# Kernel optimization log

Measured on AMD Instinct MI355X. Metric: run time of the kernel, lower is better.

The kernel has to match this reference:

```python
import jax, jax.numpy as jnp
import numpy as np
from jax import lax


def _conv3d(x, w, b, circular=False):
    # x: (B,C,D,H,W), w: (O,I,kd,kh,kw)
    if circular:
        x = jnp.pad(x, ((0, 0), (0, 0), (1, 1), (1, 1), (1, 1)), mode='wrap')
    y = lax.conv_general_dilated(x, w, (1, 1, 1), 'VALID',
                                 dimension_numbers=('NCDHW', 'OIDHW', 'NCDHW'))
    return y + b[None, :, None, None, None]


def _inorm(x):
    # InstanceNorm3d, affine=False, eps=1e-5, biased variance over spatial dims
    mu = jnp.mean(x, axis=(2, 3, 4), keepdims=True)
    var = jnp.var(x, axis=(2, 3, 4), keepdims=True)
    return (x - mu) * lax.rsqrt(var + 1e-5)


def _gelu(x):
    return jax.nn.gelu(x, approximate=False)


def _r6_to_matrix(r6):
    eps = 1e-7
    v1 = r6[..., :3]
    v1 = v1 / (jnp.linalg.norm(v1, axis=-1, keepdims=True) + eps)
    v2 = r6[..., 3:]
    v2 = v2 - jnp.sum(v2 * v1, -1, keepdims=True) * v1
    v2 = v2 / (jnp.linalg.norm(v2, axis=-1, keepdims=True) + eps)
    v3 = jnp.cross(v1, v2)
    det = jnp.linalg.det(jnp.stack([v1, v2, v3], axis=-2))
    v3 = jnp.where(det[..., None] < 0, -v3, v3)
    return jnp.stack([v1, v2, v3], axis=-2)


def _ensure_matrix(R):
    def fnorm(v):
        return v / jnp.maximum(jnp.linalg.norm(v, axis=-1, keepdims=True), 1e-12)
    v1 = fnorm(R[..., 0, :] + 1e-6)
    v2 = R[..., 1, :]
    v2 = fnorm(v2 - jnp.sum(v2 * v1, -1, keepdims=True) * v1 + 1e-6)
    v3 = jnp.cross(v1, v2)
    det = jnp.linalg.det(jnp.stack([v1, v2, v3], axis=-2))
    v3 = jnp.where(det[..., None] < 0, -v3, v3)
    Rn = jnp.stack([v1, v2, v3], axis=-2)
    Rt = jnp.swapaxes(Rn, -2, -1)
    return 0.5 * (Rn + Rt @ Rn @ Rt)


def _rotate(X, R):
    # X: (bd, nh, L, hd); R: (nh, 3, 3). Pads hd to a multiple of 3, rotates
    # each 3-vector group by R^T-on-the-right (X_rot = X @ R^T).
    hd = X.shape[-1]
    pad = (-hd) % 3
    Xp = jnp.pad(X, ((0, 0), (0, 0), (0, 0), (0, pad))) if pad else X
    nv = Xp.shape[-1] // 3
    Xr = Xp.reshape(Xp.shape[:-1] + (nv, 3))
    Y = jnp.einsum('bhlvi,hji->bhlvj', Xr, R).reshape(Xp.shape)
    return Y[..., :hd] if pad else Y


def _forward(x, pos_emb, qkv_w, qkv_b, lp_w1, lp_b1, lp_w2, lp_b2,
             mod_w1, mod_b1, mod_w2, mod_b2, pa_w, pa_b,
             proj_w, proj_b, pos_bias_w, pos_bias_b,
             A_d, A_h, A_w, R_d, R_h, R_w, t_d, t_h, t_w):
    B, C, D, H, W = x.shape
    nh = pa_w.shape[0]
    hd = C // nh
    scale = hd ** -0.5

    # PositionalProcessing (identical for all three axial passes)
    lf = _conv3d(pos_emb, lp_w1, lp_b1, circular=True)
    lf = _conv3d(_gelu(_inorm(lf)), lp_w2, lp_b2)
    m = _conv3d(lf, mod_w1, mod_b1)
    m = jax.nn.sigmoid(_conv3d(_gelu(_inorm(m)), mod_w2, mod_b2))
    x_mod = x * m                                   # (B,C,D,H,W)
    pa = _gelu(_inorm(_conv3d(pos_emb, pa_w, pa_b)))  # (B,nh,D,H,W)

    def axial(comp, perm, inv_perm, A, R, t):
        xp = jnp.transpose(x_mod, perm)             # (B, a, b, C, L)
        Bp, a, b, _, L = xp.shape
        bd = Bp * a * b
        xf = jnp.swapaxes(xp.reshape(bd, C, L), 1, 2)  # (bd, L, C)
        qkv = (xf @ qkv_w.T + qkv_b).reshape(bd, L, 3, nh, hd)
        qkv = jnp.transpose(qkv, (2, 0, 3, 1, 4))
        q, k, v = qkv[0], qkv[1], qkv[2]
        R_qk = _r6_to_matrix(A[0].astype(jnp.float32))  # (nh,3,3), same for all bd
        R_v = _ensure_matrix(R[0])                      # (nh,3,3)
        q_r, k_r, v_r = _rotate(q, R_qk), _rotate(k, R_qk), _rotate(v, R_v)
        # axis positions: linspace on one coordinate component
        pos = jnp.zeros((L, 3), x.dtype).at[:, comp].set(jnp.linspace(-1.0, 1.0, L))
        pos_t = pos[None] + t[0]                        # (nh, L, 3)
        rel = pos_t[:, :, None, :] - pos_t[:, None, :, :]  # (nh, L, L, 3)
        bias = jnp.einsum('hqkc,c->hqk', rel, pos_bias_w[0]) + pos_bias_b[0]
        pa_p = jnp.transpose(pa, perm).reshape(bd, nh, L)
        attn = jnp.einsum('bhqd,bhkd->bhqk', q_r, k_r) * scale
        attn = jax.nn.softmax(attn + pa_p[..., None] + bias[None], axis=-1)
        out = jnp.einsum('bhqk,bhkd->bhqd', attn, v_r)
        out = jnp.transpose(out, (0, 2, 1, 3)).reshape(Bp, a, b, L, C)
        return jnp.transpose(out, inv_perm)             # back to (B,C,D,H,W)

    out = (axial(2, (0, 3, 4, 1, 2), (0, 4, 3, 1, 2), A_d, R_d, t_d)
           + axial(1, (0, 2, 4, 1, 3), (0, 4, 1, 3, 2), A_h, R_h, t_h)
           + axial(0, (0, 2, 3, 1, 4), (0, 4, 1, 2, 3), A_w, R_w, t_w))
    return jnp.einsum('oc,bcdhw->bodhw', proj_w[:, :, 0, 0, 0], out) + proj_b[None, :, None, None, None]


def setup_inputs() -> dict:
    key = jax.random.key(0)
    B, C, D, H, W, nh = 2, 128, 32, 32, 32, 8
    ks = jax.random.split(key, 24)

    def n(k, shape, s=0.05):
        return (jax.random.normal(k, shape) * s).astype(jnp.float32)

    def r6(k):
        k1, k2 = jax.random.split(k)
        v1 = jax.random.normal(k1, (1, nh, 3))
        v1 = v1 / jnp.linalg.norm(v1, axis=-1, keepdims=True)
        v2 = jax.random.normal(k2, (1, nh, 3))
        v2 = v2 - jnp.sum(v2 * v1, -1, keepdims=True) * v1
        v2 = v2 / jnp.linalg.norm(v2, axis=-1, keepdims=True)
        return jnp.concatenate([v1, v2], -1).astype(jnp.float32)

    eye = jnp.broadcast_to(jnp.eye(3, dtype=jnp.float32), (1, nh, 3, 3))
    return {
        'x': jax.random.normal(ks[0], (B, C, D, H, W), jnp.float32),
        'pos_emb': jax.random.normal(ks[1], (B, C, D, H, W), jnp.float32),
        'qkv_w': n(ks[2], (3 * C, C)), 'qkv_b': n(ks[3], (3 * C,)),
        'lp_w1': n(ks[4], (C, C, 3, 3, 3), 0.02), 'lp_b1': n(ks[5], (C,)),
        'lp_w2': n(ks[6], (C, C, 1, 1, 1)), 'lp_b2': n(ks[7], (C,)),
        'mod_w1': n(ks[8], (C, C, 1, 1, 1)), 'mod_b1': n(ks[9], (C,)),
        'mod_w2': n(ks[10], (C, C, 1, 1, 1)), 'mod_b2': n(ks[11], (C,)),
        'pa_w': n(ks[12], (nh, C, 1, 1, 1)), 'pa_b': n(ks[13], (nh,)),
        'proj_w': n(ks[14], (C, C, 1, 1, 1)), 'proj_b': n(ks[15], (C,)),
        'pos_bias_w': n(ks[16], (1, 3), 0.5), 'pos_bias_b': n(ks[17], (1,)),
        'A_d': r6(ks[18]), 'A_h': r6(ks[19]), 'A_w': r6(ks[20]),
        'R_d': eye, 'R_h': eye, 'R_w': eye,
        't_d': n(ks[21], (1, nh, 1, 3), 0.01),
        't_h': n(ks[22], (1, nh, 1, 3), 0.01),
        't_w': n(ks[23], (1, nh, 1, 3), 0.01),
    }


def reference(x, pos_emb, qkv_w, qkv_b, lp_w1, lp_b1, lp_w2, lp_b2,
              mod_w1, mod_b1, mod_w2, mod_b2, pa_w, pa_b,
              proj_w, proj_b, pos_bias_w, pos_bias_b,
              A_d, A_h, A_w, R_d, R_h, R_w, t_d, t_h, t_w):
    return _forward(x, pos_emb, qkv_w, qkv_b, lp_w1, lp_b1, lp_w2, lp_b2,
                    mod_w1, mod_b1, mod_w2, mod_b2, pa_w, pa_b,
                    proj_w, proj_b, pos_bias_w, pos_bias_b,
                    A_d, A_h, A_w, R_d, R_h, R_w, t_d, t_h, t_w)
```

## Files before the change

kernel.cpp:

```cpp
#include <hip/hip_runtime.h>
#include <cstdint>
#include <cstddef>


#define NTOK 65536
#define SPAT 32768

#define WS_R0     0ull
#define WS_A0     0ull
#define WS_A1     4194304ull
#define WS_MPREB  8388608ull
#define WS_A2     8388608ull
#define WS_XTOKB  12582912ull
#define WS_INT    16777216ull
#define WS_QKVH   20971520ull
#define WS_CONVP  33554432ull
#define WS_QKVP   33775616ull
#define WS_WCP    33800192ull
#define WS_MODW2P 33808384ull
#define WS_PROJP  33816576ull
#define WS_BC     33824768ull
#define WS_RBUF   33824896ull
#define WS_PS     33825328ull
#define WS_PSS    33956400ull
#define WS_MU1    34087472ull
#define WS_RS1    34087728ull
#define WS_MU2    34087984ull
#define WS_RS2    34088240ull

typedef __attribute__((ext_vector_type(8))) short short8;
typedef __attribute__((ext_vector_type(4))) float f32x4;
typedef __attribute__((ext_vector_type(16))) float f32x16;

__device__ __forceinline__ float gelu_f(float x) {
  float u = 0.79788456080286536f * (x + 0.044715f * x * x * x);
  u = fminf(u, 40.0f);
  float e = __expf(2.0f * u);
  float t = (e - 1.0f) / (e + 1.0f);
  return 0.5f * x * (1.0f + t);
}
__device__ __forceinline__ float sigmoid_f(float x) {
  return 1.0f / (1.0f + __expf(-x));
}
__device__ __forceinline__ unsigned short f2bf(float x) {
  unsigned int u = __float_as_uint(x);
  unsigned int r = u + 0x7fffu + ((u >> 16) & 1u);
  return (unsigned short)(r >> 16);
}
__device__ __forceinline__ float bf2f(unsigned short u) {
  return __uint_as_float(((unsigned int)u) << 16);
}
__device__ __forceinline__ void bf16x16_load(const unsigned short* p, float* f) {
  const uint4 a = *(const uint4*)p;
  const uint4 b = *(const uint4*)(p + 8);
  const unsigned int w[8] = {a.x, a.y, a.z, a.w, b.x, b.y, b.z, b.w};
  #pragma unroll
  for (int i = 0; i < 8; ++i) {
    f[2 * i] = __uint_as_float(w[i] << 16);
    f[2 * i + 1] = __uint_as_float(w[i] & 0xffff0000u);
  }
}
__device__ __forceinline__ void bf16x8_load(const unsigned short* p, float* f) {
  const uint4 a = *(const uint4*)p;
  const unsigned int w[4] = {a.x, a.y, a.z, a.w};
  #pragma unroll
  for (int i = 0; i < 4; ++i) {
    f[2 * i] = __uint_as_float(w[i] << 16);
    f[2 * i + 1] = __uint_as_float(w[i] & 0xffff0000u);
  }
}
__device__ __forceinline__ void gload_lds16(const void* g, void* l) {
  __builtin_amdgcn_global_load_lds(
      (const __attribute__((address_space(1))) unsigned int*)g,
      (__attribute__((address_space(3))) unsigned int*)l, 16, 0, 0);
}
__device__ __forceinline__ float dot3(const float* a, const float* b) {
  return a[0] * b[0] + a[1] * b[1] + a[2] * b[2];
}
__device__ __forceinline__ void cross3(const float* a, const float* b, float* c) {
  c[0] = a[1] * b[2] - a[2] * b[1];
  c[1] = a[2] * b[0] - a[0] * b[2];
  c[2] = a[0] * b[1] - a[1] * b[0];
}

__device__ void r6_to_matrix(const float* r6, float* R) {
  float v1[3] = {r6[0], r6[1], r6[2]};
  float n1 = sqrtf(dot3(v1, v1));
  float inv1 = 1.0f / (n1 + 1e-7f);
  v1[0] *= inv1; v1[1] *= inv1; v1[2] *= inv1;
  float v2[3] = {r6[3], r6[4], r6[5]};
  float d = dot3(v2, v1);
  v2[0] -= d * v1[0]; v2[1] -= d * v1[1]; v2[2] -= d * v1[2];
  float n2 = sqrtf(dot3(v2, v2));
  float inv2 = 1.0f / (n2 + 1e-7f);
  v2[0] *= inv2; v2[1] *= inv2; v2[2] *= inv2;
  float v3[3]; cross3(v1, v2, v3);
  float cx[3]; cross3(v2, v3, cx);
  float det = dot3(v1, cx);
  if (det < 0.0f) { v3[0] = -v3[0]; v3[1] = -v3[1]; v3[2] = -v3[2]; }
  R[0] = v1[0]; R[1] = v1[1]; R[2] = v1[2];
  R[3] = v2[0]; R[4] = v2[1]; R[5] = v2[2];
  R[6] = v3[0]; R[7] = v3[1]; R[8] = v3[2];
}

__device__ void ensure_matrix(const float* Rin, float* Ro) {
  float a[3] = {Rin[0] + 1e-6f, Rin[1] + 1e-6f, Rin[2] + 1e-6f};
  float na = fmaxf(sqrtf(dot3(a, a)), 1e-12f);
  float v1[3] = {a[0] / na, a[1] / na, a[2] / na};
  float b0[3] = {Rin[3], Rin[4], Rin[5]};
  float d = dot3(b0, v1);
  float bb[3] = {b0[0] - d * v1[0] + 1e-6f, b0[1] - d * v1[1] + 1e-6f, b0[2] - d * v1[2] + 1e-6f};
  float nb = fmaxf(sqrtf(dot3(bb, bb)), 1e-12f);
  float v2[3] = {bb[0] / nb, bb[1] / nb, bb[2] / nb};
  float v3[3]; cross3(v1, v2, v3);
  float cx[3]; cross3(v2, v3, cx);
  float det = dot3(v1, cx);
  if (det < 0.0f) { v3[0] = -v3[0]; v3[1] = -v3[1]; v3[2] = -v3[2]; }
  float Rn[9] = {v1[0], v1[1], v1[2], v2[0], v2[1], v2[2], v3[0], v3[1], v3[2]};
  float T1[9], T2[9];
  for (int i = 0; i < 3; ++i)
    for (int j = 0; j < 3; ++j) {
      float s = 0.f;
      for (int k = 0; k < 3; ++k) s += Rn[k * 3 + i] * Rn[k * 3 + j];
      T1[i * 3 + j] = s;
    }
  for (int i = 0; i < 3; ++i)
    for (int j = 0; j < 3; ++j) {
      float s = 0.f;
      for (int k = 0; k < 3; ++k) s += T1[i * 3 + k] * Rn[j * 3 + k];
      T2[i * 3 + j] = s;
    }
  for (int i = 0; i < 9; ++i) Ro[i] = 0.5f * (Rn[i] + T2[i]);
}

__device__ __forceinline__ void rot16(const float* R, const float* x, float* y) {
  #pragma unroll
  for (int g = 0; g < 5; ++g) {
    float a = x[3 * g], b = x[3 * g + 1], c = x[3 * g + 2];
    y[3 * g + 0] = R[0] * a + R[1] * b + R[2] * c;
    y[3 * g + 1] = R[3] * a + R[4] * b + R[5] * c;
    y[3 * g + 2] = R[6] * a + R[7] * b + R[8] * c;
  }
  y[15] = R[0] * x[15];
}

__global__ __launch_bounds__(256) void prep_transpose_kernel(
    const float* __restrict__ lp_w1, const float* __restrict__ qkv_w,
    const float* __restrict__ mod_w1, const float* __restrict__ lp_w2,
    const float* __restrict__ lp_b2, const float* __restrict__ mod_b1,
    const float* __restrict__ mod_w2, const float* __restrict__ proj_w,
    const float* __restrict__ Ad, const float* __restrict__ Ah,
    const float* __restrict__ Aw, const float* __restrict__ Rd,
    const float* __restrict__ Rh, const float* __restrict__ Rw,
    const float* __restrict__ x, const float* __restrict__ pe,
    unsigned short* __restrict__ convP, unsigned short* __restrict__ qkvP,
    unsigned short* __restrict__ WcP, unsigned short* __restrict__ modw2P,
    unsigned short* __restrict__ projP, float* __restrict__ bc,
    float* __restrict__ Rbuf, unsigned short* __restrict__ xtokb,
    unsigned short* __restrict__ inT) {
  __shared__ float lds[32][132];
  if (blockIdx.x < 256) {
    int gid = blockIdx.x * 256 + threadIdx.x;
    for (int f = gid; f < 442368; f += 65536) {
      int e = f & 7;
      int co = (f >> 3) & 127;
      int rest = f >> 10;
      int l4 = rest & 3;
      int ks = (rest >> 2) & 3;
      int dxt = rest >> 4;
      int dx = dxt % 3;
      int tap = dxt / 3;
      int dz = tap / 3, dy = tap % 3;
      int ci = ks * 32 + l4 * 8 + e;
      convP[f] = f2bf(lp_w1[(co * 128 + ci) * 27 + dz * 9 + dy * 3 + dx]);
    }
    if (gid < 49152) qkvP[gid] = f2bf(qkv_w[gid]);
    if (gid < 16384) {
      modw2P[gid] = f2bf(mod_w2[gid]);
      projP[gid] = f2bf(proj_w[gid]);
      int o = gid >> 7, i = gid & 127;
      float s = 0.f;
      for (int c = 0; c < 128; ++c) s += mod_w1[o * 128 + c] * lp_w2[c * 128 + i];
      WcP[gid] = f2bf(s);
    }
    if (gid < 128) {
      float s = 0.f;
      for (int c = 0; c < 128; ++c) s += mod_w1[gid * 128 + c] * lp_b2[c];
      bc[gid] = s + mod_b1[gid];
    }
    if (blockIdx.x == 0 && threadIdx.x >= 224 && threadIdx.x < 248) {
      int tid = threadIdx.x - 224;
      int ax = tid >> 3, h = tid & 7;
      const float* A = (ax == 0) ? Ad : ((ax == 1) ? Ah : Aw);
      const float* R = (ax == 0) ? Rd : ((ax == 1) ? Rh : Rw);
      float Rq[9], Rv[9];
      r6_to_matrix(A + h * 6, Rq);
      ensure_matrix(R + h * 9, Rv);
      float* dst = Rbuf + (ax * 8 + h) * 18;
      for (int i = 0; i < 9; ++i) { dst[i] = Rq[i]; dst[9 + i] = Rv[i]; }
    }
    return;
  }
  int blk = blockIdx.x - 256;
  int b = blk >> 10;
  int dh = blk & 1023;
  int tid = threadIdx.x;
  size_t planebase = ((size_t)b << 22) + ((size_t)dh << 5);
  size_t tb = ((size_t)blk) << 5;
  #pragma unroll
  for (int r = 0; r < 16; ++r) {
    int idx = r * 256 + tid;
    int ci = idx >> 5, w = idx & 31;
    lds[w][ci] = x[planebase + ((size_t)ci << 15) + w];
  }
  __syncthreads();
  #pragma unroll
  for (int r = 0; r < 16; ++r) {
    int idx = r * 256 + tid;
    int w = idx >> 7, ci = idx & 127;
    xtokb[(tb + w) * 128 + ci] = f2bf(lds[w][ci]);
  }
  __syncthreads();
  #pragma unroll
  for (int r = 0; r < 16; ++r) {
    int idx = r * 256 + tid;
    int ci = idx >> 5, w = idx & 31;
    lds[w][ci] = pe[planebase + ((size_t)ci << 15) + w];
  }
  __syncthreads();
  #pragma unroll
  for (int r = 0; r < 16; ++r) {
    int idx = r * 256 + tid;
    int w = idx >> 7, ci = idx & 127;
    inT[(tb + w) * 128 + ci] = f2bf(lds[w][ci]);
  }
}

__global__ __launch_bounds__(256, 4) void conv_mfma_kernel(
    const unsigned short* __restrict__ inT, const unsigned short* __restrict__ Bp,
    const float* __restrict__ b1, unsigned short* __restrict__ out,
    float* __restrict__ ps, float* __restrict__ pss) {
  __shared__ unsigned short Als[16384];
  __shared__ float sumb[128];
  __shared__ float sqb[128];
  const int orig = blockIdx.x;
  const int blk = ((orig & 7) << 7) + (orig >> 3);
  const int b = blk >> 9, d = (blk >> 4) & 31, hg = blk & 15;
  const int h0 = hg << 1;
  const int tid = threadIdx.x;
  const int lane = tid & 63;
  const int wid = tid >> 6;
  const int l15 = lane & 15, l4 = lane >> 4;

  f32x4 acc[4][2];
  #pragma unroll
  for (int mt = 0; mt < 4; ++mt)
    #pragma unroll
    for (int nt = 0; nt < 2; ++nt)
      #pragma unroll
      for (int r = 0; r < 4; ++r) acc[mt][nt][r] = 0.f;

  int mw[4], mhh[4];
  #pragma unroll
  for (int mt = 0; mt < 4; ++mt) {
    int m = mt * 16 + l15;
    mhh[mt] = m >> 5;
    mw[mt] = m & 31;
  }
  const size_t tokbase = ((size_t)b << 15) + ((size_t)d << 10) + ((size_t)h0 << 5);

  auto stage = [&](int dz) {
    const int zr = (d + dz + 31) & 31;
    #pragma unroll
    for (int p = 0; p < 8; ++p) {
      const int g = p * 256 + tid;
      const int tok = g >> 4, gi = g & 15;
      const int r = tok >> 5, w = tok & 31;
      const int yr = (h0 + r + 31) & 31;
      const size_t srcbyte = ((((size_t)b << 15) + ((size_t)zr << 10) + ((size_t)yr << 5) + w) << 8)
                             + (size_t)((gi ^ (w & 7)) << 4);
      gload_lds16((const char*)inT + srcbyte, (char*)Als + (size_t)g * 16);
    }
  };

  auto compute = [&](int dz) {
    #pragma unroll
    for (int dy = 0; dy < 3; ++dy) {
      const int tap = dz * 3 + dy;
      #pragma unroll
      for (int dx = 0; dx < 3; ++dx) {
        int abase[4], asw[4];
        #pragma unroll
        for (int mt = 0; mt < 4; ++mt) {
          const int wsft = (mw[mt] + dx + 31) & 31;
          const int stok = (mhh[mt] + dy) * 32 + wsft;
          abase[mt] = stok * 256;
          asw[mt] = (wsft & 7) << 4;
        }
        #pragma unroll
        for (int ks = 0; ks < 4; ++ks) {
          const int k2 = (ks * 32 + l4 * 8) * 2;
          const int bbase = (((tap * 3 + dx) * 4 + ks) * 4 + l4) * 1024;
          short8 afr[4], bfr[2];
          #pragma unroll
          for (int nt = 0; nt < 2; ++nt) {
            const int co = wid * 32 + nt * 16 + l15;
            bfr[nt] = *(const short8*)(Bp + bbase + co * 8);
          }
          #pragma unroll
          for (int mt = 0; mt < 4; ++mt)
            afr[mt] = *(const short8*)((const char*)Als + abase[mt] + (k2 ^ asw[mt]));
          __builtin_amdgcn_s_setprio(1);
          #pragma unroll
          for (int mt = 0; mt < 4; ++mt)
            #pragma unroll
            for (int nt = 0; nt < 2; ++nt)
              acc[mt][nt] = __builtin_amdgcn_mfma_f32_16x16x32_bf16(afr[mt], bfr[nt],
                                                                    acc[mt][nt], 0, 0, 0);
          __builtin_amdgcn_s_setprio(0);
        }
      }
    }
  };

  for (int dz = 0; dz < 3; ++dz) {
    stage(dz);
    __syncthreads();
    compute(dz);
    if (dz < 2) __syncthreads();
  }

  #pragma unroll
  for (int nt = 0; nt < 2; ++nt) {
    const int co = wid * 32 + nt * 16 + l15;
    const float bias = b1[co];
    float s = 0.f, q = 0.f;
    #pragma unroll
    for (int mt = 0; mt < 4; ++mt) {
      #pragma unroll
      for (int r = 0; r < 4; ++r) {
        const int m = mt * 16 + l4 * 4 + r;
        const float v = acc[mt][nt][r] + bias;
        out[(tokbase + m) * 128 + co] = f2bf(v);
        s += v; q += v * v;
      }
    }
    s += __shfl_xor(s, 16); s += __shfl_xor(s, 32);
    q += __shfl_xor(q, 16); q += __shfl_xor(q, 32);
    if (l4 == 0) { sumb[co] = s; sqb[co] = q; }
  }
  __syncthreads();
  if (tid < 128) {
    ps[blk * 128 + tid] = sumb[tid];
    pss[blk * 128 + tid] = sqb[tid];
  }
}

__global__ __launch_bounds__(64) void stats_final_kernel(
    const float* __restrict__ ps, const float* __restrict__ pss,
    float* __restrict__ mu, float* __restrict__ rs, int nb) {
  const int pair = blockIdx.x;
  const int b = pair >> 7, c = pair & 127;
  const int lane = threadIdx.x;
  float s = 0.f, ss = 0.f;
  for (int j = lane; j < nb; j += 64) {
    const int idx = ((b * nb + j) << 7) + c;
    s += ps[idx];
    ss += pss[idx];
  }
  #pragma unroll
  for (int o = 32; o > 0; o >>= 1) {
    s += __shfl_xor(s, o);
    ss += __shfl_xor(ss, o);
  }
  if (lane == 0) {
    float m = s * (1.0f / 32768.0f);
    float v = ss * (1.0f / 32768.0f) - m * m;
    mu[pair] = m;
    rs[pair] = rsqrtf(v + 1e-5f);
  }
}

template <int PRE, int AB16, int POST, int STATS>
__global__ __launch_bounds__(256) void gemm_mfma_kernel(
    const void* __restrict__ Avoid, const unsigned short* __restrict__ Wp,
    const float* __restrict__ bias, void* __restrict__ Yvoid, int O,
    const float* __restrict__ mu, const float* __restrict__ rs,
    const unsigned short* __restrict__ xtb, float* __restrict__ ps,
    float* __restrict__ pss) {
  __shared__ float sumb[128][2];
  __shared__ float sqb[128][2];
  const int tid = threadIdx.x;
  const int lane = tid & 63, wid = tid >> 6;
  const int wm = wid >> 1, wn = wid & 1;
  const int l15 = lane & 15, l4 = lane >> 4;
  const int og = blockIdx.x * 128;
  const int t0 = blockIdx.y * 128;
  const int bidx = t0 >> 15;
  const float* Af = (const float*)Avoid;
  const unsigned short* Ab = (const unsigned short*)Avoid;
  float* Yf = (float*)Yvoid;
  unsigned short* Yb = (unsigned short*)Yvoid;

  f32x4 acc[4][4];
  #pragma unroll
  for (int mt = 0; mt < 4; ++mt)
    #pragma unroll
    for (int nt = 0; nt < 4; ++nt)
      #pragma unroll
      for (int r = 0; r < 4; ++r) acc[mt][nt][r] = 0.f;

  #pragma unroll
  for (int ks = 0; ks < 4; ++ks) {
    const int kb = ks * 32 + l4 * 8;
    short8 a[4], bfr[4];
    float4 m0, m1, r0, r1;
    if constexpr (PRE == 1) {
      m0 = *(const float4*)(mu + bidx * 128 + kb);
      m1 = *(const float4*)(mu + bidx * 128 + kb + 4);
      r0 = *(const float4*)(rs + bidx * 128 + kb);
      r1 = *(const float4*)(rs + bidx * 128 + kb + 4);
    }
    #pragma unroll
    for (int mt = 0; mt < 4; ++mt) {
      const int tok = t0 + wm * 64 + mt * 16 + l15;
      float v[16];
      bool have = false;
      if constexpr (AB16 == 1) {
        if constexpr (PRE == 1) {
          bf16x16_load(Ab + (size_t)tok * 128 + kb, v);
          have = true;
        } else {
          a[mt] = *(const short8*)(Ab + (size_t)tok * 128 + kb);
        }
      } else {
        const float* ap = Af + (size_t)tok * 128 + kb;
        float4 v0 = *(const float4*)ap;
        float4 v1 = *(const float4*)(ap + 4);
        v[0] = v0.x; v[1] = v0.y; v[2] = v0.z; v[3] = v0.w;
        v[4] = v1.x; v[5] = v1.y; v[6] = v1.z; v[7] = v1.w;
        have = true;
      }
      if (have) {
        if constexpr (PRE == 1) {
          const float mm[8] = {m0.x, m0.y, m0.z, m0.w, m1.x, m1.y, m1.z, m1.w};
          const float rr[8] = {r0.x, r0.y, r0.z, r0.w, r1.x, r1.y, r1.z, r1.w};
          #pragma unroll
          for (int j = 0; j < 8; ++j) v[j] = gelu_f((v[j] - mm[j]) * rr[j]);
        }
        short8 t;
        #pragma unroll
        for (int j = 0; j < 8; ++j) t[j] = (short)f2bf(v[j]);
        a[mt] = t;
      }
    }
    #pragma unroll
    for (int nt = 0; nt < 4; ++nt) {
      const int o = og + wn * 64 + nt * 16 + l15;
      bfr[nt] = *(const short8*)(Wp + (size_t)o * 128 + kb);
    }
    #pragma unroll
    for (int mt = 0; mt < 4; ++mt)
      #pragma unroll
      for (int nt = 0; nt < 4; ++nt)
        acc[mt][nt] = __builtin_amdgcn_mfma_f32_16x16x32_bf16(a[mt], bfr[nt], acc[mt][nt], 0, 0, 0);
  }

  #pragma unroll
  for (int nt = 0; nt < 4; ++nt) {
    const int o = og + wn * 64 + nt * 16 + l15;
    const float bb = bias[o];
    float s = 0.f, q = 0.f;
    #pragma unroll
    for (int mt = 0; mt < 4; ++mt) {
      #pragma unroll
      for (int r = 0; r < 4; ++r) {
        const int t = t0 + wm * 64 + mt * 16 + l4 * 4 + r;
        const float v = acc[mt][nt][r] + bb;
        if constexpr (POST == 0) {
          Yf[(size_t)t * O + o] = v;
        } else if constexpr (POST == 2) {
          Yb[(size_t)t * O + o] = f2bf(v);
        }
        if constexpr (STATS) { s += v; q += v * v; }
      }
    }
    if constexpr (STATS) {
      s += __shfl_xor(s, 16); s += __shfl_xor(s, 32);
      q += __shfl_xor(q, 16); q += __shfl_xor(q, 32);
      if (l4 == 0) { sumb[o - og][wm] = s; sqb[o - og][wm] = q; }
    }
  }
  if constexpr (STATS) {
    __syncthreads();
    if (tid < 128) {
      ps[blockIdx.y * 128 + tid] = sumb[tid][0] + sumb[tid][1];
      pss[blockIdx.y * 128 + tid] = sqb[tid][0] + sqb[tid][1];
    }
  }
}

__global__ __launch_bounds__(256) void gateqkv_mfma_kernel(
    const unsigned short* __restrict__ mpreb, const unsigned short* __restrict__ modw2P,
    const float* __restrict__ mod_b2, const unsigned short* __restrict__ xtb,
    const unsigned short* __restrict__ qkvP, const float* __restrict__ qkv_b,
    unsigned short* __restrict__ qkvt, const float* __restrict__ mu,
    const float* __restrict__ rs) {
  __shared__ char ga[32768];
  __shared__ char xm[32768];
  const int tid = threadIdx.x;
  const int lane = tid & 63, wid = tid >> 6;
  const int wm = wid >> 1, wn = wid & 1;
  const int l15 = lane & 15, l4 = lane >> 4;
  const int t0 = blockIdx.x * 128;
  const int bidx = t0 >> 15;

  #pragma unroll
  for (int r = 0; r < 8; ++r) {
    const int c = r * 256 + tid;
    const int tl = c >> 4;
    const int kc = (c & 15) * 8;
    float v[8];
    bf16x8_load(mpreb + (size_t)(t0 + tl) * 128 + kc, v);
    const float4 m0 = *(const float4*)(mu + bidx * 128 + kc);
    const float4 m1 = *(const float4*)(mu + bidx * 128 + kc + 4);
    const float4 r0 = *(const float4*)(rs + bidx * 128 + kc);
    const float4 r1 = *(const float4*)(rs + bidx * 128 + kc + 4);
    const float mm[8] = {m0.x, m0.y, m0.z, m0.w, m1.x, m1.y, m1.z, m1.w};
    const float rr[8] = {r0.x, r0.y, r0.z, r0.w, r1.x, r1.y, r1.z, r1.w};
    short8 t;
    #pragma unroll
    for (int j = 0; j < 8; ++j) t[j] = (short)f2bf(gelu_f((v[j] - mm[j]) * rr[j]));
    *(short8*)(ga + tl * 256 + ((kc * 2) ^ ((tl & 7) << 4))) = t;
  }
  __syncthreads();

  f32x4 acc[4][4];
  #pragma unroll
  for (int mt = 0; mt < 4; ++mt)
    #pragma unroll
    for (int nt = 0; nt < 4; ++nt)
      #pragma unroll
      for (int r = 0; r < 4; ++r) acc[mt][nt][r] = 0.f;

  #pragma unroll
  for (int ks = 0; ks < 4; ++ks) {
    const int kb = ks * 32 + l4 * 8;
    short8 a[4], bfr[4];
    #pragma unroll
    for (int mt = 0; mt < 4; ++mt) {
      const int tl = wm * 64 + mt * 16 + l15;
      a[mt] = *(const short8*)(ga + tl * 256 + ((kb * 2) ^ ((tl & 7) << 4)));
    }
    #pragma unroll
    for (int nt = 0; nt < 4; ++nt) {
      const int o = wn * 64 + nt * 16 + l15;
      bfr[nt] = *(const short8*)(modw2P + (size_t)o * 128 + kb);
    }
    #pragma unroll
    for (int mt = 0; mt < 4; ++mt)
      #pragma unroll
      for (int nt = 0; nt < 4; ++nt)
        acc[mt][nt] = __builtin_amdgcn_mfma_f32_16x16x32_bf16(a[mt], bfr[nt], acc[mt][nt], 0, 0, 0);
  }
  #pragma unroll
  for (int nt = 0; nt < 4; ++nt) {
    const int o = wn * 64 + nt * 16 + l15;
    const float bb = mod_b2[o];
    #pragma unroll
    for (int mt = 0; mt < 4; ++mt) {
      #pragma unroll
      for (int r = 0; r < 4; ++r) {
        const int tl = wm * 64 + mt * 16 + l4 * 4 + r;
        const int t = t0 + tl;
        const float v = sigmoid_f(acc[mt][nt][r] + bb) * bf2f(xtb[(size_t)t * 128 + o]);
        *(unsigned short*)(xm + tl * 256 + ((o * 2) ^ ((tl & 7) << 4))) = f2bf(v);
      }
    }
  }
  __syncthreads();

  for (int c = 0; c < 3; ++c) {
    #pragma unroll
    for (int mt = 0; mt < 4; ++mt)
      #pragma unroll
      for (int nt = 0; nt < 4; ++nt)
        #pragma unroll
        for (int r = 0; r < 4; ++r) acc[mt][nt][r] = 0.f;
    #pragma unroll
    for (int ks = 0; ks < 4; ++ks) {
      const int kb = ks * 32 + l4 * 8;
      short8 a[4], bfr[4];
      #pragma unroll
      for (int mt = 0; mt < 4; ++mt) {
        const int tl = wm * 64 + mt * 16 + l15;
        a[mt] = *(const short8*)(xm + tl * 256 + ((kb * 2) ^ ((tl & 7) << 4)));
      }
      #pragma unroll
      for (int nt = 0; nt < 4; ++nt) {
        const int o = c * 128 + wn * 64 + nt * 16 + l15;
        bfr[nt] = *(const short8*)(qkvP + (size_t)o * 128 + kb);
      }
      #pragma unroll
      for (int mt = 0; mt < 4; ++mt)
        #pragma unroll
        for (int nt = 0; nt < 4; ++nt)
          acc[mt][nt] = __builtin_amdgcn_mfma_f32_16x16x32_bf16(a[mt], bfr[nt], acc[mt][nt], 0, 0, 0);
    }
    #pragma unroll
    for (int nt = 0; nt < 4; ++nt) {
      const int o = c * 128 + wn * 64 + nt * 16 + l15;
      const float bb = qkv_b[o];
      const int hsub = (o & 127) >> 4, ch = o & 15;
      #pragma unroll
      for (int mt = 0; mt < 4; ++mt) {
        #pragma unroll
        for (int r = 0; r < 4; ++r) {
          const int t = t0 + wm * 64 + mt * 16 + l4 * 4 + r;
          qkvt[(size_t)t * 384 + hsub * 48 + c * 16 + ch] = f2bf(acc[mt][nt][r] + bb);
        }
      }
    }
  }
}

__global__ __launch_bounds__(256) void proj_mfma_kernel(
    const unsigned short* __restrict__ A0b, const unsigned short* __restrict__ A1b,
    const unsigned short* __restrict__ A2b, const unsigned short* __restrict__ Wp,
    const float* __restrict__ bias, float* __restrict__ out) {
  const int tid = threadIdx.x;
  const int lane = tid & 63, wid = tid >> 6;
  const int wm = wid >> 1, wn = wid & 1;
  const int l15 = lane & 15, l4 = lane >> 4;
  const int t0 = blockIdx.x * 128;

  f32x4 acc[4][4];
  #pragma unroll
  for (int mt = 0; mt < 4; ++mt)
    #pragma unroll
    for (int nt = 0; nt < 4; ++nt)
      #pragma unroll
      for (int r = 0; r < 4; ++r) acc[mt][nt][r] = 0.f;

  #pragma unroll
  for (int ks = 0; ks < 4; ++ks) {
    const int kb = ks * 32 + l4 * 8;
    short8 a[4], bfr[4];
    #pragma unroll
    for (int mt = 0; mt < 4; ++mt) {
      const int o = wm * 64 + mt * 16 + l15;
      a[mt] = *(const short8*)(Wp + (size_t)o * 128 + kb);
    }
    #pragma unroll
    for (int nt = 0; nt < 4; ++nt) {
      const int tok = t0 + wn * 64 + nt * 16 + l15;
      const size_t off = (size_t)tok * 128 + kb;
      short8 s0 = *(const short8*)(A0b + off);
      short8 s1 = *(const short8*)(A1b + off);
      short8 s2 = *(const short8*)(A2b + off);
      short8 r;
      #pragma unroll
      for (int i = 0; i < 8; ++i) {
        float f = bf2f((unsigned short)s0[i]) + bf2f((unsigned short)s1[i]) +
                  bf2f((unsigned short)s2[i]);
        r[i] = (short)f2bf(f);
      }
      bfr[nt] = r;
    }
    #pragma unroll
    for (int mt = 0; mt < 4; ++mt)
      #pragma unroll
      for (int nt = 0; nt < 4; ++nt)
        acc[mt][nt] = __builtin_amdgcn_mfma_f32_16x16x32_bf16(a[mt], bfr[nt], acc[mt][nt], 0, 0, 0);
  }

  #pragma unroll
  for (int nt = 0; nt < 4; ++nt) {
    const int tok = t0 + wn * 64 + nt * 16 + l15;
    const int dhw = tok & 32767, bB = tok >> 15;
    #pragma unroll
    for (int mt = 0; mt < 4; ++mt) {
      #pragma unroll
      for (int r = 0; r < 4; ++r) {
        const int o = wm * 64 + mt * 16 + l4 * 4 + r;
        out[((size_t)(bB * 128 + o) << 15) + dhw] = acc[mt][nt][r] + bias[o];
      }
    }
  }
}

__global__ __launch_bounds__(512) void attn_mfma_kernel(
    const unsigned short* __restrict__ qkvt, const float* __restrict__ Rbuf,
    const float* __restrict__ pbw, unsigned short* __restrict__ a0,
    unsigned short* __restrict__ a1, unsigned short* __restrict__ a2) {
  __shared__ unsigned short rows[32 * 392];
  __shared__ unsigned short Vt[8][16 * 40];
  __shared__ float Ot[8][32 * 20];
  const int axial = blockIdx.y;
  const int seq = blockIdx.x;
  unsigned short* dstbuf = (axial == 0) ? a0 : ((axial == 1) ? a1 : a2);
  const int tid = threadIdx.x;
  const int lane = tid & 63, head = tid >> 6;
  const int tok = lane & 31, hi = lane >> 5;
  const int b = seq >> 10, rem = seq & 1023;
  const int u = rem >> 5, v = rem & 31;
  int base, stride, comp;
  if (axial == 0)      { base = (b << 15) + (u << 5) + v;         stride = 1024; comp = 2; }
  else if (axial == 1) { base = (b << 15) + (u << 10) + v;        stride = 32;   comp = 1; }
  else                 { base = (b << 15) + (u << 10) + (v << 5); stride = 1;    comp = 0; }

  #pragma unroll
  for (int p = 0; p < 3; ++p) {
    const int c = p * 512 + tid;
    const int r = c / 48, cw = c - r * 48;
    const size_t src = ((size_t)base + (size_t)r * stride) * 384 + (size_t)cw * 8;
    *(uint4*)((char*)rows + r * 784 + cw * 16) = *(const uint4*)(qkvt + src);
  }
  __syncthreads();

  const float* Rp = Rbuf + (axial * 8 + head) * 18;
  const float rq00 = fabsf(Rp[0]);
  const unsigned short* myrow = rows + tok * 392 + head * 48;
  short8 aq = *(const short8*)(myrow + hi * 8);
  short8 ak = *(const short8*)(myrow + 16 + hi * 8);
  short8 av = *(const short8*)(myrow + 32 + hi * 8);
  if (hi) {
    aq[7] = (short)f2bf(bf2f((unsigned short)aq[7]) * rq00);
    ak[7] = (short)f2bf(bf2f((unsigned short)ak[7]) * rq00);
  }
  #pragma unroll
  for (int e = 0; e < 8; ++e) Vt[head][(hi * 8 + e) * 40 + tok] = (unsigned short)av[e];

  f32x16 sacc;
  #pragma unroll
  for (int r = 0; r < 16; ++r) sacc[r] = 0.f;
  sacc = __builtin_amdgcn_mfma_f32_32x32x16_bf16(ak, aq, sacc, 0, 0, 0);
  const float wb = pbw[comp];
  float p[16];
  float mmax = -1e30f;
  #pragma unroll
  for (int r = 0; r < 16; ++r) {
    const int kk = (r & 3) + 4 * hi + 8 * (r >> 2);
    const float lin = -1.0f + (2.0f / 31.0f) * (float)kk;
    p[r] = sacc[r] * 0.25f - lin * wb;
    mmax = fmaxf(mmax, p[r]);
  }
  mmax = fmaxf(mmax, __shfl_xor(mmax, 32));
  float sum = 0.f;
  #pragma unroll
  for (int r = 0; r < 16; ++r) { p[r] = expf(p[r] - mmax); sum += p[r]; }
  sum += __shfl_xor(sum, 32);
  const float inv = 1.0f / sum;
  #pragma unroll
  for (int r = 0; r < 16; ++r) p[r] *= inv;
  unsigned pk[8], sw[8];
  #pragma unroll
  for (int j = 0; j < 8; ++j) {
    unsigned r_;
    asm("v_cvt_pk_bf16_f32 %0, %1, %2" : "=v"(r_) : "v"(p[2 * j]), "v"(p[2 * j + 1]));
    pk[j] = r_;
  }
  #pragma unroll
  for (int j = 0; j < 8; ++j) sw[j] = (unsigned)__shfl_xor((int)pk[j], 32);
  uint4 Fu, Gu;
  Fu.x = hi ? sw[2] : pk[0];
  Fu.y = hi ? sw[3] : pk[1];
  Fu.z = hi ? pk[2] : sw[0];
  Fu.w = hi ? pk[3] : sw[1];
  Gu.x = hi ? sw[6] : pk[4];
  Gu.y = hi ? sw[7] : pk[5];
  Gu.z = hi ? pk[6] : sw[4];
  Gu.w = hi ? pk[7] : sw[5];
  short8 Pf = *(short8*)&Fu;
  short8 Pg = *(short8*)&Gu;
  const unsigned short* vrow = Vt[head] + (tok & 15) * 40;
  short8 Bv0 = *(const short8*)(vrow + hi * 8);
  short8 Bv1 = *(const short8*)(vrow + 16 + hi * 8);
  f32x16 oacc;
  #pragma unroll
  for (int r = 0; r < 16; ++r) oacc[r] = 0.f;
  oacc = __builtin_amdgcn_mfma_f32_32x32x16_bf16(Pf, Bv0, oacc, 0, 0, 0);
  oacc = __builtin_amdgcn_mfma_f32_32x32x16_bf16(Pg, Bv1, oacc, 0, 0, 0);
  if (tok < 16) {
    #pragma unroll
    for (int r = 0; r < 16; ++r) {
      const int q = (r & 3) + 4 * hi + 8 * (r >> 2);
      Ot[head][q * 20 + tok] = oacc[r];
    }
  }
  if (lane < 32) {
    float o16[16], y16[16], Rv[9];
    #pragma unroll
    for (int j = 0; j < 16; ++j) o16[j] = Ot[head][lane * 20 + j];
    #pragma unroll
    for (int i = 0; i < 9; ++i) Rv[i] = Rp[9 + i];
    rot16(Rv, o16, y16);
    unsigned outw[8];
    #pragma unroll
    for (int j = 0; j < 8; ++j)
      outw[j] = ((unsigned)f2bf(y16[2 * j + 1]) << 16) | (unsigned)f2bf(y16[2 * j]);
    const size_t t2 = (size_t)base + (size_t)lane * stride;
    unsigned short* dst = dstbuf + t2 * 128 + head * 16;
    uint4 o0 = {outw[0], outw[1], outw[2], outw[3]};
    uint4 o1 = {outw[4], outw[5], outw[6], outw[7]};
    *(uint4*)dst = o0;
    *(uint4*)(dst + 8) = o1;
  }
}

extern "C" void kernel_launch(void* const* d_in, const int* in_sizes, int n_in,
                              void* d_out, int out_size, void* d_ws, size_t ws_size,
                              hipStream_t stream) {
  const float* x       = (const float*)d_in[0];
  const float* pos_emb = (const float*)d_in[1];
  const float* qkv_w   = (const float*)d_in[2];
  const float* qkv_b   = (const float*)d_in[3];
  const float* lp_w1   = (const float*)d_in[4];
  const float* lp_b1   = (const float*)d_in[5];
  const float* lp_w2   = (const float*)d_in[6];
  const float* lp_b2   = (const float*)d_in[7];
  const float* mod_w1  = (const float*)d_in[8];
  const float* mod_b1  = (const float*)d_in[9];
  const float* mod_w2  = (const float*)d_in[10];
  const float* mod_b2  = (const float*)d_in[11];
  const float* proj_w  = (const float*)d_in[14];
  const float* proj_b  = (const float*)d_in[15];
  const float* pbw     = (const float*)d_in[16];
  const float* Ad      = (const float*)d_in[18];
  const float* Ah      = (const float*)d_in[19];
  const float* Aw      = (const float*)d_in[20];
  const float* Rd      = (const float*)d_in[21];
  const float* Rh      = (const float*)d_in[22];
  const float* Rw      = (const float*)d_in[23];

  float* ws = (float*)d_ws;
  unsigned short* lfb    = (unsigned short*)(ws + WS_R0);
  unsigned short* A0b    = (unsigned short*)(ws + WS_A0);
  unsigned short* A1b    = (unsigned short*)(ws + WS_A1);
  unsigned short* A2b    = (unsigned short*)(ws + WS_A2);
  unsigned short* mpreb  = (unsigned short*)(ws + WS_MPREB);
  unsigned short* xtokb  = (unsigned short*)(ws + WS_XTOKB);
  unsigned short* inT    = (unsigned short*)(ws + WS_INT);
  unsigned short* qkvt   = (unsigned short*)(ws + WS_QKVH);
  unsigned short* convP  = (unsigned short*)(ws + WS_CONVP);
  unsigned short* qkvP   = (unsigned short*)(ws + WS_QKVP);
  unsigned short* WcP    = (unsigned short*)(ws + WS_WCP);
  unsigned short* modw2P = (unsigned short*)(ws + WS_MODW2P);
  unsigned short* projP  = (unsigned short*)(ws + WS_PROJP);
  float* bc     = ws + WS_BC;
  float* Rbuf   = ws + WS_RBUF;
  float* ps     = ws + WS_PS;
  float* pss    = ws + WS_PSS;
  float* mu1    = ws + WS_MU1;
  float* rs1    = ws + WS_RS1;
  float* mu2    = ws + WS_MU2;
  float* rs2    = ws + WS_RS2;

  prep_transpose_kernel<<<2304, 256, 0, stream>>>(
      lp_w1, qkv_w, mod_w1, lp_w2, lp_b2, mod_b1, mod_w2, proj_w,
      Ad, Ah, Aw, Rd, Rh, Rw, x, pos_emb,
      convP, qkvP, WcP, modw2P, projP, bc, Rbuf, xtokb, inT);
  conv_mfma_kernel<<<1024, 256, 0, stream>>>(inT, convP, lp_b1, lfb, ps, pss);
  stats_final_kernel<<<256, 64, 0, stream>>>(ps, pss, mu1, rs1, 512);
  gemm_mfma_kernel<1, 1, 2, 1><<<dim3(1, 512), 256, 0, stream>>>(
      lfb, WcP, bc, mpreb, 128, mu1, rs1, nullptr, ps, pss);
  stats_final_kernel<<<256, 64, 0, stream>>>(ps, pss, mu2, rs2, 256);
  gateqkv_mfma_kernel<<<512, 256, 0, stream>>>(
      mpreb, modw2P, mod_b2, xtokb, qkvP, qkv_b, qkvt, mu2, rs2);
  attn_mfma_kernel<<<dim3(2048, 3), 512, 0, stream>>>(qkvt, Rbuf, pbw, A0b, A1b, A2b);
  proj_mfma_kernel<<<512, 256, 0, stream>>>(A0b, A1b, A2b, projP, proj_b, (float*)d_out);
}
```

Baseline: 228.0 us.

## Stage normalized GELU A-tile in swizzled LDS and alias attention LDS buffers

Replaces the templated GEMM with a dedicated Wc kernel. It normalizes, applies GELU to and converts the 128x128 activation tile to bf16 once into XOR-swizzled shared memory. Previously both column-half waves recomputed GELU on the same A fragments straight from global memory. The attention kernel now reuses the row-staging LDS buffer for the output transpose scratch, which shrinks its shared-memory footprint to allow more resident blocks. This costs an extra block barrier.

```diff
diff --git a/kernel.cpp b/kernel.cpp
--- a/kernel.cpp
+++ b/kernel.cpp
@@ -49,16 +49,6 @@
 }
 __device__ __forceinline__ float bf2f(unsigned short u) {
   return __uint_as_float(((unsigned int)u) << 16);
-}
-__device__ __forceinline__ void bf16x16_load(const unsigned short* p, float* f) {
-  const uint4 a = *(const uint4*)p;
-  const uint4 b = *(const uint4*)(p + 8);
-  const unsigned int w[8] = {a.x, a.y, a.z, a.w, b.x, b.y, b.z, b.w};
-  #pragma unroll
-  for (int i = 0; i < 8; ++i) {
-    f[2 * i] = __uint_as_float(w[i] << 16);
-    f[2 * i + 1] = __uint_as_float(w[i] & 0xffff0000u);
-  }
 }
 __device__ __forceinline__ void bf16x8_load(const unsigned short* p, float* f) {
   const uint4 a = *(const uint4*)p;
@@ -381,26 +371,40 @@
   }
 }
 
-template <int PRE, int AB16, int POST, int STATS>
-__global__ __launch_bounds__(256) void gemm_mfma_kernel(
-    const void* __restrict__ Avoid, const unsigned short* __restrict__ Wp,
-    const float* __restrict__ bias, void* __restrict__ Yvoid, int O,
+__global__ __launch_bounds__(256) void wc_mfma_kernel(
+    const unsigned short* __restrict__ lfb, const unsigned short* __restrict__ WcP,
+    const float* __restrict__ bc, unsigned short* __restrict__ mpreb,
     const float* __restrict__ mu, const float* __restrict__ rs,
-    const unsigned short* __restrict__ xtb, float* __restrict__ ps,
-    float* __restrict__ pss) {
+    float* __restrict__ ps, float* __restrict__ pss) {
+  __shared__ char ga[32768];
   __shared__ float sumb[128][2];
   __shared__ float sqb[128][2];
   const int tid = threadIdx.x;
   const int lane = tid & 63, wid = tid >> 6;
   const int wm = wid >> 1, wn = wid & 1;
   const int l15 = lane & 15, l4 = lane >> 4;
-  const int og = blockIdx.x * 128;
-  const int t0 = blockIdx.y * 128;
+  const int t0 = blockIdx.x * 128;
   const int bidx = t0 >> 15;
-  const float* Af = (const float*)Avoid;
-  const unsigned short* Ab = (const unsigned short*)Avoid;
-  float* Yf = (float*)Yvoid;
-  unsigned short* Yb = (unsigned short*)Yvoid;
+
+  #pragma unroll
+  for (int r = 0; r < 8; ++r) {
+    const int c = r * 256 + tid;
+    const int tl = c >> 4;
+    const int kc = (c & 15) * 8;
+    float v[8];
+    bf16x8_load(lfb + (size_t)(t0 + tl) * 128 + kc, v);
+    const float4 m0 = *(const float4*)(mu + bidx * 128 + kc);
+    const float4 m1 = *(const float4*)(mu + bidx * 128 + kc + 4);
+    const float4 r0 = *(const float4*)(rs + bidx * 128 + kc);
+    const float4 r1 = *(const float4*)(rs + bidx * 128 + kc + 4);
+    const float mm[8] = {m0.x, m0.y, m0.z, m0.w, m1.x, m1.y, m1.z, m1.w};
+    const float rr[8] = {r0.x, r0.y, r0.z, r0.w, r1.x, r1.y, r1.z, r1.w};
+    short8 t;
+    #pragma unroll
+    for (int j = 0; j < 8; ++j) t[j] = (short)f2bf(gelu_f((v[j] - mm[j]) * rr[j]));
+    *(short8*)(ga + tl * 256 + ((kc * 2) ^ ((tl & 7) << 4))) = t;
+  }
+  __syncthreads();
 
   f32x4 acc[4][4];
   #pragma unroll
@@ -414,50 +418,15 @@
   for (int ks = 0; ks < 4; ++ks) {
     const int kb = ks * 32 + l4 * 8;
     short8 a[4], bfr[4];
-    float4 m0, m1, r0, r1;
-    if constexpr (PRE == 1) {
-      m0 = *(const float4*)(mu + bidx * 128 + kb);
-      m1 = *(const float4*)(mu + bidx * 128 + kb + 4);
-      r0 = *(const float4*)(rs + bidx * 128 + kb);
-      r1 = *(const float4*)(rs + bidx * 128 + kb + 4);
-    }
     #pragma unroll
     for (int mt = 0; mt < 4; ++mt) {
-      const int tok = t0 + wm * 64 + mt * 16 + l15;
-      float v[16];
-      bool have = false;
-      if constexpr (AB16 == 1) {
-        if constexpr (PRE == 1) {
-          bf16x16_load(Ab + (size_t)tok * 128 + kb, v);
-          have = true;
-        } else {
-          a[mt] = *(const short8*)(Ab + (size_t)tok * 128 + kb);
-        }
-      } else {
-        const float* ap = Af + (size_t)tok * 128 + kb;
-        float4 v0 = *(const float4*)ap;
-        float4 v1 = *(const float4*)(ap + 4);
-        v[0] = v0.x; v[1] = v0.y; v[2] = v0.z; v[3] = v0.w;
-        v[4] = v1.x; v[5] = v1.y; v[6] = v1.z; v[7] = v1.w;
-        have = true;
-      }
-      if (have) {
-        if constexpr (PRE == 1) {
-          const float mm[8] = {m0.x, m0.y, m0.z, m0.w, m1.x, m1.y, m1.z, m1.w};
-          const float rr[8] = {r0.x, r0.y, r0.z, r0.w, r1.x, r1.y, r1.z, r1.w};
-          #pragma unroll
-          for (int j = 0; j < 8; ++j) v[j] = gelu_f((v[j] - mm[j]) * rr[j]);
-        }
-        short8 t;
-        #pragma unroll
-        for (int j = 0; j < 8; ++j) t[j] = (short)f2bf(v[j]);
-        a[mt] = t;
-      }
+      const int tl = wm * 64 + mt * 16 + l15;
+      a[mt] = *(const short8*)(ga + tl * 256 + ((kb * 2) ^ ((tl & 7) << 4)));
     }
     #pragma unroll
     for (int nt = 0; nt < 4; ++nt) {
-      const int o = og + wn * 64 + nt * 16 + l15;
-      bfr[nt] = *(const short8*)(Wp + (size_t)o * 128 + kb);
+      const int o = wn * 64 + nt * 16 + l15;
+      bfr[nt] = *(const short8*)(WcP + (size_t)o * 128 + kb);
     }
     #pragma unroll
     for (int mt = 0; mt < 4; ++mt)
@@ -468,8 +437,8 @@
 
   #pragma unroll
   for (int nt = 0; nt < 4; ++nt) {
-    const int o = og + wn * 64 + nt * 16 + l15;
-    const float bb = bias[o];
+    const int o = wn * 64 + nt * 16 + l15;
+    const float bb = bc[o];
     float s = 0.f, q = 0.f;
     #pragma unroll
     for (int mt = 0; mt < 4; ++mt) {
@@ -477,26 +446,18 @@
       for (int r = 0; r < 4; ++r) {
         const int t = t0 + wm * 64 + mt * 16 + l4 * 4 + r;
         const float v = acc[mt][nt][r] + bb;
-        if constexpr (POST == 0) {
-          Yf[(size_t)t * O + o] = v;
-        } else if constexpr (POST == 2) {
-          Yb[(size_t)t * O + o] = f2bf(v);
-        }
-        if constexpr (STATS) { s += v; q += v * v; }
+        mpreb[(size_t)t * 128 + o] = f2bf(v);
+        s += v; q += v * v;
       }
     }
-    if constexpr (STATS) {
-      s += __shfl_xor(s, 16); s += __shfl_xor(s, 32);
-      q += __shfl_xor(q, 16); q += __shfl_xor(q, 32);
-      if (l4 == 0) { sumb[o - og][wm] = s; sqb[o - og][wm] = q; }
-    }
-  }
-  if constexpr (STATS) {
-    __syncthreads();
-    if (tid < 128) {
-      ps[blockIdx.y * 128 + tid] = sumb[tid][0] + sumb[tid][1];
-      pss[blockIdx.y * 128 + tid] = sqb[tid][0] + sqb[tid][1];
-    }
+    s += __shfl_xor(s, 16); s += __shfl_xor(s, 32);
+    q += __shfl_xor(q, 16); q += __shfl_xor(q, 32);
+    if (l4 == 0) { sumb[o][wm] = s; sqb[o][wm] = q; }
+  }
+  __syncthreads();
+  if (tid < 128) {
+    ps[blockIdx.x * 128 + tid] = sumb[tid][0] + sumb[tid][1];
+    pss[blockIdx.x * 128 + tid] = sqb[tid][0] + sqb[tid][1];
   }
 }
 
@@ -693,9 +654,10 @@
     const unsigned short* __restrict__ qkvt, const float* __restrict__ Rbuf,
     const float* __restrict__ pbw, unsigned short* __restrict__ a0,
     unsigned short* __restrict__ a1, unsigned short* __restrict__ a2) {
-  __shared__ unsigned short rows[32 * 392];
+  __shared__ char shb[32 * 784];
   __shared__ unsigned short Vt[8][16 * 40];
-  __shared__ float Ot[8][32 * 20];
+  unsigned short* rows = (unsigned short*)shb;
+  float* OtA = (float*)shb;
   const int axial = blockIdx.y;
   const int seq = blockIdx.x;
   unsigned short* dstbuf = (axial == 0) ? a0 : ((axial == 1) ? a1 : a2);
@@ -730,6 +692,7 @@
   }
   #pragma unroll
   for (int e = 0; e < 8; ++e) Vt[head][(hi * 8 + e) * 40 + tok] = (unsigned short)av[e];
+  __syncthreads();
 
   f32x16 sacc;
   #pragma unroll
@@ -785,13 +748,13 @@
     #pragma unroll
     for (int r = 0; r < 16; ++r) {
       const int q = (r & 3) + 4 * hi + 8 * (r >> 2);
-      Ot[head][q * 20 + tok] = oacc[r];
+      OtA[head * 640 + q * 20 + tok] = oacc[r];
     }
   }
   if (lane < 32) {
     float o16[16], y16[16], Rv[9];
     #pragma unroll
-    for (int j = 0; j < 16; ++j) o16[j] = Ot[head][lane * 20 + j];
+    for (int j = 0; j < 16; ++j) o16[j] = OtA[head * 640 + lane * 20 + j];
     #pragma unroll
     for (int i = 0; i < 9; ++i) Rv[i] = Rp[9 + i];
     rot16(Rv, o16, y16);
@@ -862,8 +825,7 @@
       convP, qkvP, WcP, modw2P, projP, bc, Rbuf, xtokb, inT);
   conv_mfma_kernel<<<1024, 256, 0, stream>>>(inT, convP, lp_b1, lfb, ps, pss);
   stats_final_kernel<<<256, 64, 0, stream>>>(ps, pss, mu1, rs1, 512);
-  gemm_mfma_kernel<1, 1, 2, 1><<<dim3(1, 512), 256, 0, stream>>>(
-      lfb, WcP, bc, mpreb, 128, mu1, rs1, nullptr, ps, pss);
+  wc_mfma_kernel<<<512, 256, 0, stream>>>(lfb, WcP, bc, mpreb, mu1, rs1, ps, pss);
   stats_final_kernel<<<256, 64, 0, stream>>>(ps, pss, mu2, rs2, 256);
   gateqkv_mfma_kernel<<<512, 256, 0, stream>>>(
       mpreb, modw2P, mod_b2, xtokb, qkvP, qkv_b, qkvt, mu2, rs2);
```

After: 219.6 us, median of 3. 3.7% less time.
